# Performance work log

Hardware: AMD Instinct MI355X
Metric: run time of the kernel (lower is better)

## Reference

```python
import jax, jax.numpy as jnp
import numpy as np

B, C, INNER, H, W = 32, 256, 128, 32, 32
EPS = 1e-5


def _conv1x1(x, w):
    # x: (B, Cin, H, W); w: (Cout, Cin) -> (B, Cout, H, W)
    return jnp.einsum('bchw,oc->bohw', x, w)


def _attend(q, k, v):
    # q,k: (B, D, H, W); v: (B, C, H, W)
    b, d, h, w = q.shape
    n = h * w
    qf = q.reshape(b, d, n).transpose(0, 2, 1)            # (B, N, D)
    kf = k.reshape(b, d, n).transpose(0, 2, 1)            # (B, N, D)
    vf = v.reshape(b, v.shape[1], n).transpose(0, 2, 1)   # (B, N, C)
    scale = 1.0 / jnp.sqrt(jnp.asarray(d, qf.dtype))
    attn = jax.nn.softmax(jnp.einsum('bnd,bmd->bnm', qf, kf) * scale, axis=-1)
    of = jnp.einsum('bnm,bmc->bnc', attn, vf)             # (B, N, C)
    return of.transpose(0, 2, 1).reshape(b, -1, h, w)


def _layernorm(x, w, b):
    # Normalize over (C, H, W) jointly; affine params broadcast from (C,1,1).
    mu = jnp.mean(x, axis=(1, 2, 3), keepdims=True)
    var = jnp.mean(jnp.square(x - mu), axis=(1, 2, 3), keepdims=True)
    return (x - mu) * jax.lax.rsqrt(var + EPS) * w[None] + b[None]


def setup_inputs() -> dict:
    key = jax.random.key(0)
    ks = jax.random.split(key, 10)
    s = 0.02
    return {
        'fs': jax.random.normal(ks[0], (B, C, H, W), jnp.float32),
        'fi': jax.random.normal(ks[1], (B, C, H, W), jnp.float32),
        'qs_w': jax.random.normal(ks[2], (INNER, C), jnp.float32) * s,
        'ks_w': jax.random.normal(ks[3], (INNER, C), jnp.float32) * s,
        'vs_w': jax.random.normal(ks[4], (C, C), jnp.float32) * s,
        'qi_w': jax.random.normal(ks[5], (INNER, C), jnp.float32) * s,
        'ki_w': jax.random.normal(ks[6], (INNER, C), jnp.float32) * s,
        'vi_w': jax.random.normal(ks[7], (C, C), jnp.float32) * s,
        'fuse_w': jax.random.normal(ks[8], (C, 2 * C), jnp.float32) * s,
        'fuse_b': jnp.zeros((C,), jnp.float32),
        'ln_s_w': jnp.ones((C, 1, 1), jnp.float32),
        'ln_s_b': jnp.zeros((C, 1, 1), jnp.float32),
        'ln_i_w': jnp.ones((C, 1, 1), jnp.float32),
        'ln_i_b': jnp.zeros((C, 1, 1), jnp.float32),
    }


def reference(fs, fi, qs_w, ks_w, vs_w, qi_w, ki_w, vi_w,
              fuse_w, fuse_b, ln_s_w, ln_s_b, ln_i_w, ln_i_b):
    # sketch queries attend over image keys/values
    s2i = _attend(_conv1x1(fs, qs_w), _conv1x1(fi, ki_w), _conv1x1(fi, vi_w))
    # image queries attend over sketch keys/values
    i2s = _attend(_conv1x1(fi, qi_w), _conv1x1(fs, ks_w), _conv1x1(fs, vs_w))

    def fuse(x):
        return jax.nn.relu(_conv1x1(x, fuse_w) + fuse_b[None, :, None, None])

    fs_out = _layernorm(fuse(jnp.concatenate([fs, i2s], axis=1)) + fs, ln_s_w, ln_s_b)
    fi_out = _layernorm(fuse(jnp.concatenate([fi, s2i], axis=1)) + fi, ln_i_w, ln_i_b)
    return (fs_out, fi_out)
```

## Files before the change

### kernel.cpp

```cpp
#include <hip/hip_runtime.h>

typedef unsigned short u16;
typedef unsigned int   u32;

#define B_   32
#define C_   256
#define N_   1024
#define CN_  (C_*N_)
#define EPS_ 1e-5f

typedef __attribute__((ext_vector_type(8))) short  short8;
typedef __attribute__((ext_vector_type(4))) float  f32x4;

__device__ __forceinline__ float b2f(u16 u){
  union { u32 u; float f; } c; c.u = ((u32)u) << 16; return c.f;
}
__device__ __forceinline__ u16 f2b(float f){
  union { float f; u32 u; } c; c.f = f;
  u32 u = c.u;
  return (u16)((u + 0x7FFFu + ((u >> 16) & 1u)) >> 16);
}

struct F4v { float v[4]; };

__device__ __forceinline__ F4v ld4g(const void* p, long i, int bf){
  F4v r;
  if (bf){
    ushort4 u = *(const ushort4*)((const u16*)p + i);
    r.v[0]=b2f(u.x); r.v[1]=b2f(u.y); r.v[2]=b2f(u.z); r.v[3]=b2f(u.w);
  } else {
    float4 f = *(const float4*)((const float*)p + i);
    r.v[0]=f.x; r.v[1]=f.y; r.v[2]=f.z; r.v[3]=f.w;
  }
  return r;
}
__device__ __forceinline__ float ld1g(const void* p, long i, int bf){
  return bf ? b2f(((const u16*)p)[i]) : ((const float*)p)[i];
}
__device__ __forceinline__ void st1g(void* p, long i, float v, int bf){
  if (bf) ((u16*)p)[i] = f2b(v); else ((float*)p)[i] = v;
}
__device__ __forceinline__ void st4g(void* p, long i, const float* v, int bf){
  if (bf){
    ushort4 u;
    u.x=f2b(v[0]); u.y=f2b(v[1]); u.z=f2b(v[2]); u.w=f2b(v[3]);
    *(ushort4*)((u16*)p + i) = u;
  } else {
    *(float4*)((float*)p + i) = make_float4(v[0],v[1],v[2],v[3]);
  }
}
__device__ __forceinline__ int sniff_bf(const void* lnw){
  return (*(const u32*)lnw == 0x3F803F80u) ? 1 : 0;
}

__global__ __launch_bounds__(256) void k_prep_w(
    const void* qs, const void* ks, const void* vs,
    const void* qi, const void* ki, const void* vi,
    const void* fw, const void* lnw,
    u16* __restrict__ Wcat, u16* __restrict__ fuseWb, float* __restrict__ stats)
{
  const int bf = sniff_bf(lnw);
  if (blockIdx.x == 0 && threadIdx.x < 128) stats[threadIdx.x] = 0.0f;
  const long idx = ((long)blockIdx.x*256 + threadIdx.x) * 4;
  if (idx < 262144){
    const int side = (int)(idx >> 17);
    const int rem  = (int)(idx & 131071);
    const int row  = rem >> 8, col = rem & 255;
    const void* src; int r2;
    if (row < 128)      { src = side ? qi : qs; r2 = row; }
    else if (row < 256) { src = side ? ki : ks; r2 = row - 128; }
    else                { src = side ? vi : vs; r2 = row - 256; }
    F4v v = ld4g(src, (long)r2*256 + col, bf);
    ushort4 u; u.x=f2b(v.v[0]); u.y=f2b(v.v[1]); u.z=f2b(v.v[2]); u.w=f2b(v.v[3]);
    *(ushort4*)&Wcat[idx] = u;
  } else {
    const long j = idx - 262144;
    F4v v = ld4g(fw, j, bf);
    ushort4 u; u.x=f2b(v.v[0]); u.y=f2b(v.v[1]); u.z=f2b(v.v[2]); u.w=f2b(v.v[3]);
    *(ushort4*)&fuseWb[j] = u;
  }
}

__global__ __launch_bounds__(256) void k_prep_t(
    const void* fs, const void* fi, const void* lnw, u16* __restrict__ Ft)
{
  const int bf = sniff_bf(lnw);
  const int nt = blockIdx.x, ct = blockIdx.y, bs = blockIdx.z;
  const int b = bs >> 1, side = bs & 1;
  const void* F = side ? fi : fs;
  const int t = threadIdx.x;
  __shared__ u16 T[64][72];
  const int c0 = ct << 6, n0 = nt << 6;
  const int nc = (t & 15) << 2, cl = t >> 4;
  #pragma unroll
  for (int p = 0; p < 4; p++){
    const int c = cl + (p << 4);
    F4v v = ld4g(F, ((long)b*C_ + c0 + c)*N_ + n0 + nc, bf);
    T[nc  ][c] = f2b(v.v[0]);
    T[nc+1][c] = f2b(v.v[1]);
    T[nc+2][c] = f2b(v.v[2]);
    T[nc+3][c] = f2b(v.v[3]);
  }
  __syncthreads();
  const int nl = t >> 2, cc = (t & 3) << 4;
  float4 x0 = *(const float4*)&T[nl][cc];
  float4 x1 = *(const float4*)&T[nl][cc + 8];
  u16* dst = Ft + ((long)bs << 18) + (long)(n0 + nl)*256 + c0 + cc;
  *(float4*)dst = x0;
  *(float4*)(dst + 8) = x1;
}

__global__ __launch_bounds__(256) void k_proj(
    const u16* __restrict__ Wcat, const u16* __restrict__ Ft,
    u16* __restrict__ QKp, u16* __restrict__ Vp)
{
  const int nt = blockIdx.x;
  const int ot = blockIdx.y;
  const int bs = blockIdx.z;
  const int side = bs & 1;
  const int t = threadIdx.x;
  const int wv = t >> 6, li = t & 15, qd = (t >> 4) & 3;
  const int o0 = (ot << 7) + (wv << 5);
  const int n0 = nt << 7;

  const u16* ap = Wcat + ((long)side*512 + o0 + li)*256 + qd*8;
  const u16* bp = Ft + ((long)bs << 18) + (long)(n0 + li)*256 + qd*8;

  const f32x4 z4 = {0.f,0.f,0.f,0.f};
  f32x4 acc[2][8];
  #pragma unroll
  for (int i = 0; i < 2; i++)
    #pragma unroll
    for (int j = 0; j < 8; j++) acc[i][j] = z4;

  for (int ks = 0; ks < 8; ks++){
    const int ko = ks*32;
    short8 a0 = *(const short8*)(ap + ko);
    short8 a1 = *(const short8*)(ap + 16*256 + ko);
    short8 bfr[8];
    #pragma unroll
    for (int j = 0; j < 8; j++) bfr[j] = *(const short8*)(bp + (long)j*16*256 + ko);
    #pragma unroll
    for (int j = 0; j < 8; j++){
      acc[0][j] = __builtin_amdgcn_mfma_f32_16x16x32_bf16(a0, bfr[j], acc[0][j], 0, 0, 0);
      acc[1][j] = __builtin_amdgcn_mfma_f32_16x16x32_bf16(a1, bfr[j], acc[1][j], 0, 0, 0);
    }
  }

  if (o0 < 256){
    u16* base = QKp + ((long)bs << 18);
    #pragma unroll
    for (int mi = 0; mi < 2; mi++){
      const int ocol = o0 + mi*16 + qd*4;
      #pragma unroll
      for (int j = 0; j < 8; j++){
        const int n = n0 + j*16 + li;
        ushort4 u;
        u.x = f2b(acc[mi][j][0]); u.y = f2b(acc[mi][j][1]);
        u.z = f2b(acc[mi][j][2]); u.w = f2b(acc[mi][j][3]);
        *(ushort4*)&base[(long)n*256 + ocol] = u;
      }
    }
  } else {
    u16* base = Vp + ((long)bs << 18);
    #pragma unroll
    for (int mi = 0; mi < 2; mi++){
      #pragma unroll
      for (int j = 0; j < 8; j++){
        const int n = n0 + j*16 + li;
        #pragma unroll
        for (int r = 0; r < 4; r++){
          const int c = o0 - 256 + mi*16 + qd*4 + r;
          base[(long)c*N_ + n] = f2b(acc[mi][j][r]);
        }
      }
    }
  }
}

#define ATTN_STEP(MT, KCUR, KNXT)                                              \
{                                                                              \
  const int m0s = (MT) << 6;                                                   \
                       \
  short8 va[8];                                                                \
  {                                                                            \
    const u16* vrow = Vb + (long)(cb + li)*N_ + m0s + qd*8;                    \
    _Pragma("unroll")                                                          \
    for (int i4 = 0; i4 < 4; i4++){                                            \
      va[i4*2  ] = *(const short8*)(vrow + (long)i4*16*N_);                    \
      va[i4*2+1] = *(const short8*)(vrow + (long)i4*16*N_ + 32);               \
    }                                                                          \
  }                                                                            \
                  \
  {                                                                            \
    const int m0n = (((MT)+1) & 15) << 6;                                      \
    const u16* krow = Kb + (long)(m0n + (wv<<4) + li)*256 + qd*8;              \
    _Pragma("unroll")                                                          \
    for (int kk = 0; kk < 4; kk++)                                             \
      KNXT[kk] = *(const short8*)(krow + kk*32);                               \
  }                                                                            \
                                \
  f32x4 sf[4];                                                                 \
  sf[0]=z4; sf[1]=z4; sf[2]=z4; sf[3]=z4;                                      \
  _Pragma("unroll")                                                            \
  for (int j4 = 0; j4 < 4; j4++)                                               \
    _Pragma("unroll")                                                          \
    for (int kk = 0; kk < 4; kk++)                                             \
      sf[j4] = __builtin_amdgcn_mfma_f32_16x16x32_bf16(qf[j4][kk], KCUR[kk], sf[j4], 0, 0, 0); \
                  \
  u16 (*Pb)[72] = Pt[(MT) & 1];                                                \
  _Pragma("unroll")                                                            \
  for (int j4 = 0; j4 < 4; j4++){                                              \
    _Pragma("unroll")                                                          \
    for (int r = 0; r < 4; r++){                                               \
      float p = __expf(fminf(sf[j4][r]*scale, 60.0f));                         \
      Pb[(j4<<4) + (qd<<2) + r][(wv<<4) + li] = f2b(p);                        \
      rs[j4][r] += p;                                                          \
    }                                                                          \
  }                                                                            \
  __syncthreads();                                                             \
                                            \
  _Pragma("unroll")                                                            \
  for (int j4 = 0; j4 < 4; j4++){                                              \
    short8 pb0 = *(const short8*)&Pb[(j4<<4) + li][qd*8];                      \
    short8 pb1 = *(const short8*)&Pb[(j4<<4) + li][qd*8 + 32];                 \
    _Pragma("unroll")                                                          \
    for (int i4 = 0; i4 < 4; i4++){                                            \
      accO[i4][j4] = __builtin_amdgcn_mfma_f32_16x16x32_bf16(va[i4*2  ], pb0, accO[i4][j4], 0, 0, 0); \
      accO[i4][j4] = __builtin_amdgcn_mfma_f32_16x16x32_bf16(va[i4*2+1], pb1, accO[i4][j4], 0, 0, 0); \
    }                                                                          \
  }                                                                            \
}

__global__ __launch_bounds__(256) void k_attn(
    const u16* __restrict__ QKp, const u16* __restrict__ Vp, u16* __restrict__ AOt)
{
  const int id   = blockIdx.x;
  const int pair = id & 63;
  const int nt   = id >> 6;
  const int b  = pair >> 1, tt = pair & 1;
  const int qside = 1 - tt, kvside = tt;
  const u16* Qb = QKp + (((long)(b*2+qside)) << 18);
  const u16* Kb = QKp + (((long)(b*2+kvside)) << 18) + 128;
  const u16* Vb = Vp  + (((long)(b*2+kvside)) << 18);

  const int t  = threadIdx.x;
  const int wv = t >> 6;
  const int li = t & 15;
  const int qd = (t >> 4) & 3;
  const int n0 = nt << 6;
  const int cb = wv << 6;

  __shared__ __align__(16) u16 Pt[2][64][72];
  __shared__ float lSp[4][64];

  short8 qf[4][4];
  #pragma unroll
  for (int j4 = 0; j4 < 4; j4++){
    const u16* qrow = Qb + (long)(n0 + (j4<<4) + li)*256 + qd*8;
    #pragma unroll
    for (int kk = 0; kk < 4; kk++) qf[j4][kk] = *(const short8*)(qrow + kk*32);
  }

  const f32x4 z4 = {0.f, 0.f, 0.f, 0.f};
  f32x4 accO[4][4];
  #pragma unroll
  for (int i = 0; i < 4; i++)
    #pragma unroll
    for (int j = 0; j < 4; j++) accO[i][j] = z4;
  float rs[4][4];
  #pragma unroll
  for (int i = 0; i < 4; i++)
    #pragma unroll
    for (int r = 0; r < 4; r++) rs[i][r] = 0.0f;
  const float scale = 0.088388347648318447f;

  short8 kfA[4], kfB[4];
  {
    const u16* krow = Kb + (long)((wv<<4) + li)*256 + qd*8;
    #pragma unroll
    for (int kk = 0; kk < 4; kk++) kfA[kk] = *(const short8*)(krow + kk*32);
  }

  for (int mt2 = 0; mt2 < 16; mt2 += 2){
    ATTN_STEP(mt2,     kfA, kfB)
    ATTN_STEP(mt2 + 1, kfB, kfA)
  }

  #pragma unroll
  for (int j4 = 0; j4 < 4; j4++){
    #pragma unroll
    for (int r = 0; r < 4; r++){
      float s = rs[j4][r];
      s += __shfl_xor(s, 1, 64);
      s += __shfl_xor(s, 2, 64);
      s += __shfl_xor(s, 4, 64);
      s += __shfl_xor(s, 8, 64);
      if (li == 0) lSp[wv][(j4<<4) + (qd<<2) + r] = s;
    }
  }
  __syncthreads();
  float linv[4];
  #pragma unroll
  for (int j4 = 0; j4 < 4; j4++){
    const int q = (j4<<4) + li;
    linv[j4] = 1.0f / (lSp[0][q] + lSp[1][q] + lSp[2][q] + lSp[3][q]);
  }
  u16* aob = AOt + (((long)(b*2+tt)) << 18);
  #pragma unroll
  for (int i4 = 0; i4 < 4; i4++){
    #pragma unroll
    for (int j4 = 0; j4 < 4; j4++){
      const int n = n0 + (j4<<4) + li;
      ushort4 u;
      u.x = f2b(accO[i4][j4][0] * linv[j4]);
      u.y = f2b(accO[i4][j4][1] * linv[j4]);
      u.z = f2b(accO[i4][j4][2] * linv[j4]);
      u.w = f2b(accO[i4][j4][3] * linv[j4]);
      *(ushort4*)&aob[(long)n*256 + cb + (i4<<4) + (qd<<2)] = u;
    }
  }
}

__global__ __launch_bounds__(256) void k_fuse(
    const void* fs, const void* fi, const u16* __restrict__ fuseWb,
    const void* fbias, const u16* __restrict__ Ft, const u16* __restrict__ AOt,
    void* out, float* __restrict__ stats, const void* lnw)
{
  const int bf = sniff_bf(lnw);
  const int nt = blockIdx.x;
  const int ot = blockIdx.y;
  const int bw = blockIdx.z;
  const int b = bw >> 1, w = bw & 1;
  const void* F = w ? fi : fs;
  const int t = threadIdx.x;
  const int wv = t >> 6, li = t & 15, qd = (t >> 4) & 3;
  const int o0 = (ot << 7) + (wv << 5);
  const int n0 = nt << 7;

  const u16* ap  = fuseWb + (long)(o0 + li)*512 + qd*8;
  const u16* bp1 = Ft  + ((long)bw << 18) + (long)(n0 + li)*256 + qd*8;
  const u16* bp2 = AOt + ((long)bw << 18) + (long)(n0 + li)*256 + qd*8;

  const f32x4 z4 = {0.f,0.f,0.f,0.f};
  f32x4 acc[2][8];
  #pragma unroll
  for (int i = 0; i < 2; i++)
    #pragma unroll
    for (int j = 0; j < 8; j++) acc[i][j] = z4;

  for (int ks = 0; ks < 16; ks++){
    const u16* bp = (ks < 8) ? (bp1 + ks*32) : (bp2 + (ks-8)*32);
    const int ko = ks*32;
    short8 a0 = *(const short8*)(ap + ko);
    short8 a1 = *(const short8*)(ap + 16*512 + ko);
    short8 bfr[8];
    #pragma unroll
    for (int j = 0; j < 8; j++) bfr[j] = *(const short8*)(bp + (long)j*16*256);
    #pragma unroll
    for (int j = 0; j < 8; j++){
      acc[0][j] = __builtin_amdgcn_mfma_f32_16x16x32_bf16(a0, bfr[j], acc[0][j], 0, 0, 0);
      acc[1][j] = __builtin_amdgcn_mfma_f32_16x16x32_bf16(a1, bfr[j], acc[1][j], 0, 0, 0);
    }
  }

  __shared__ float rbuf[8];
  float s1 = 0.0f, s2 = 0.0f;
  #pragma unroll
  for (int mi = 0; mi < 2; mi++){
    float biasv[4];
    #pragma unroll
    for (int r = 0; r < 4; r++) biasv[r] = ld1g(fbias, o0 + mi*16 + qd*4 + r, bf);
    #pragma unroll
    for (int j = 0; j < 8; j++){
      const int n = n0 + j*16 + li;
      #pragma unroll
      for (int r = 0; r < 4; r++){
        const int o = o0 + mi*16 + qd*4 + r;
        const float res = ld1g(F, ((long)b*C_ + o)*N_ + n, bf);
        float y = acc[mi][j][r] + biasv[r];
        y = y > 0.0f ? y : 0.0f;
        y += res;
        s1 += y; s2 += y*y;
        st1g(out, ((long)w*B_ + b)*CN_ + (long)o*N_ + n, y, bf);
      }
    }
  }
  #pragma unroll
  for (int off = 32; off > 0; off >>= 1){
    s1 += __shfl_down(s1, off, 64);
    s2 += __shfl_down(s2, off, 64);
  }
  const int lane = t & 63;
  if (lane == 0){ rbuf[wv*2] = s1; rbuf[wv*2+1] = s2; }
  __syncthreads();
  if (t == 0){
    atomicAdd(&stats[bw*2  ], rbuf[0]+rbuf[2]+rbuf[4]+rbuf[6]);
    atomicAdd(&stats[bw*2+1], rbuf[1]+rbuf[3]+rbuf[5]+rbuf[7]);
  }
}

__global__ __launch_bounds__(256) void k_ln(
    void* out, const float* __restrict__ stats,
    const void* lsw, const void* lsb, const void* liw, const void* lib)
{
  const int bf = sniff_bf(lsw);
  const long g = ((long)blockIdx.x*256 + threadIdx.x) * 4;
  const long half = (long)B_*CN_;
  const int w = (g >= half) ? 1 : 0;
  const long rem = g - (long)w*half;
  const int b  = (int)(rem >> 18);
  const int cn = (int)(rem & (CN_-1));
  const int c  = cn >> 10;
  const float s1v = stats[(b*2+w)*2], s2v = stats[(b*2+w)*2+1];
  const float inv = 1.0f / (float)CN_;
  const float mean = s1v * inv;
  const float var  = s2v * inv - mean*mean;
  const float rstd = rsqrtf(var + EPS_);
  const float lw = ld1g(w ? liw : lsw, c, bf);
  const float lb = ld1g(w ? lib : lsb, c, bf);
  F4v x = ld4g(out, g, bf);
  float vv[4];
  #pragma unroll
  for (int j = 0; j < 4; j++) vv[j] = (x.v[j] - mean)*rstd*lw + lb;
  st4g(out, g, vv, bf);
}

extern "C" void kernel_launch(void* const* d_in, const int* in_sizes, int n_in,
                              void* d_out, int out_size, void* d_ws, size_t ws_size,
                              hipStream_t stream)
{
  const void* fs     = d_in[0];
  const void* fi     = d_in[1];
  const void* qs_w   = d_in[2];
  const void* ks_w   = d_in[3];
  const void* vs_w   = d_in[4];
  const void* qi_w   = d_in[5];
  const void* ki_w   = d_in[6];
  const void* vi_w   = d_in[7];
  const void* fuse_w = d_in[8];
  const void* fuse_b = d_in[9];
  const void* ln_s_w = d_in[10];
  const void* ln_s_b = d_in[11];
  const void* ln_i_w = d_in[12];
  const void* ln_i_b = d_in[13];

  char* ws = (char*)d_ws;
  float* stats  = (float*)ws;
  u16*   Wcat   = (u16*)(ws + 4096);
  u16*   fuseWb = (u16*)(ws + 4096 + 524288);
  u16*   Ft     = (u16*)(ws + (1u<<20));
  u16*   QKp    = (u16*)(ws + (1u<<20) + (1u<<25));
  u16*   Vp     = (u16*)(ws + (1u<<20) + 2u*(1u<<25));
  u16*   AOt    = (u16*)(ws + (1u<<20) + 3u*(1u<<25));

  k_prep_w<<<dim3(384), dim3(256), 0, stream>>>(
      qs_w, ks_w, vs_w, qi_w, ki_w, vi_w, fuse_w, ln_s_w, Wcat, fuseWb, stats);
  k_prep_t<<<dim3(16,4,64), dim3(256), 0, stream>>>(fs, fi, ln_s_w, Ft);
  k_proj<<<dim3(8,4,64), dim3(256), 0, stream>>>(Wcat, Ft, QKp, Vp);
  k_attn<<<dim3(1024), dim3(256), 0, stream>>>(QKp, Vp, AOt);
  k_fuse<<<dim3(8,2,64), dim3(256), 0, stream>>>(
      fs, fi, fuseWb, fuse_b, Ft, AOt, d_out, stats, ln_s_w);
  k_ln<<<dim3(16384), dim3(256), 0, stream>>>(
      d_out, stats, ln_s_w, ln_s_b, ln_i_w, ln_i_b);
}
```

Before: 479.8 us.

## Stage V projection stores via LDS and restructure attention loop for occupancy

The projection kernel now stages V-output tiles in shared memory and writes them back with coalesced 16-byte row stores, replacing the strided scalar transposed stores. The attention kernel stops keeping Q fragments in registers and reloads them each tile, which drops the K double buffering. It also adds launch bounds for 3 blocks per CU and remaps block ids so neighbouring blocks share a batch pair. On top of that it uses exp2 with a prescaled constant, packed bf16 conversion, s_setprio around the MFMA sections, and a raw waitcnt+barrier. The goal is higher occupancy and better memory coalescing, at the cost of repeated Q loads from global/cache and an extra LDS buffer in the projection kernel.

```diff
diff --git a/kernel.cpp b/kernel.cpp
--- a/kernel.cpp
+++ b/kernel.cpp
@@ -123,6 +123,8 @@
   const int o0 = (ot << 7) + (wv << 5);
   const int n0 = nt << 7;
 
+  __shared__ __align__(16) u16 VT[128][136];
+
   const u16* ap = Wcat + ((long)side*512 + o0 + li)*256 + qd*8;
   const u16* bp = Ft + ((long)bs << 18) + (long)(n0 + li)*256 + qd*8;
 
@@ -162,82 +164,39 @@
       }
     }
   } else {
-    u16* base = Vp + ((long)bs << 18);
     #pragma unroll
     for (int mi = 0; mi < 2; mi++){
       #pragma unroll
       for (int j = 0; j < 8; j++){
-        const int n = n0 + j*16 + li;
+        const int n = j*16 + li;
         #pragma unroll
         for (int r = 0; r < 4; r++){
-          const int c = o0 - 256 + mi*16 + qd*4 + r;
-          base[(long)c*N_ + n] = f2b(acc[mi][j][r]);
+          const int cl = (wv<<5) + mi*16 + qd*4 + r;
+          VT[cl][n] = f2b(acc[mi][j][r]);
         }
       }
     }
-  }
-}
-
-#define ATTN_STEP(MT, KCUR, KNXT)                                              \
-{                                                                              \
-  const int m0s = (MT) << 6;                                                   \
-                       \
-  short8 va[8];                                                                \
-  {                                                                            \
-    const u16* vrow = Vb + (long)(cb + li)*N_ + m0s + qd*8;                    \
-    _Pragma("unroll")                                                          \
-    for (int i4 = 0; i4 < 4; i4++){                                            \
-      va[i4*2  ] = *(const short8*)(vrow + (long)i4*16*N_);                    \
-      va[i4*2+1] = *(const short8*)(vrow + (long)i4*16*N_ + 32);               \
-    }                                                                          \
-  }                                                                            \
-                  \
-  {                                                                            \
-    const int m0n = (((MT)+1) & 15) << 6;                                      \
-    const u16* krow = Kb + (long)(m0n + (wv<<4) + li)*256 + qd*8;              \
-    _Pragma("unroll")                                                          \
-    for (int kk = 0; kk < 4; kk++)                                             \
-      KNXT[kk] = *(const short8*)(krow + kk*32);                               \
-  }                                                                            \
-                                \
-  f32x4 sf[4];                                                                 \
-  sf[0]=z4; sf[1]=z4; sf[2]=z4; sf[3]=z4;                                      \
-  _Pragma("unroll")                                                            \
-  for (int j4 = 0; j4 < 4; j4++)                                               \
-    _Pragma("unroll")                                                          \
-    for (int kk = 0; kk < 4; kk++)                                             \
-      sf[j4] = __builtin_amdgcn_mfma_f32_16x16x32_bf16(qf[j4][kk], KCUR[kk], sf[j4], 0, 0, 0); \
-                  \
-  u16 (*Pb)[72] = Pt[(MT) & 1];                                                \
-  _Pragma("unroll")                                                            \
-  for (int j4 = 0; j4 < 4; j4++){                                              \
-    _Pragma("unroll")                                                          \
-    for (int r = 0; r < 4; r++){                                               \
-      float p = __expf(fminf(sf[j4][r]*scale, 60.0f));                         \
-      Pb[(j4<<4) + (qd<<2) + r][(wv<<4) + li] = f2b(p);                        \
-      rs[j4][r] += p;                                                          \
-    }                                                                          \
-  }                                                                            \
-  __syncthreads();                                                             \
-                                            \
-  _Pragma("unroll")                                                            \
-  for (int j4 = 0; j4 < 4; j4++){                                              \
-    short8 pb0 = *(const short8*)&Pb[(j4<<4) + li][qd*8];                      \
-    short8 pb1 = *(const short8*)&Pb[(j4<<4) + li][qd*8 + 32];                 \
-    _Pragma("unroll")                                                          \
-    for (int i4 = 0; i4 < 4; i4++){                                            \
-      accO[i4][j4] = __builtin_amdgcn_mfma_f32_16x16x32_bf16(va[i4*2  ], pb0, accO[i4][j4], 0, 0, 0); \
-      accO[i4][j4] = __builtin_amdgcn_mfma_f32_16x16x32_bf16(va[i4*2+1], pb1, accO[i4][j4], 0, 0, 0); \
-    }                                                                          \
-  }                                                                            \
-}
-
-__global__ __launch_bounds__(256) void k_attn(
+    __syncthreads();
+    const int c0g = (ot - 2) << 7;
+    u16* baseV = Vp + ((long)bs << 18);
+    const int rb   = t >> 4;
+    const int c16  = t & 15;
+    #pragma unroll
+    for (int ch = 0; ch < 8; ch++){
+      const int r = rb + (ch << 4);
+      float4 x = *(const float4*)&VT[r][c16*8];
+      *(float4*)&baseV[(long)(c0g + r)*N_ + n0 + c16*8] = x;
+    }
+  }
+}
+
+__global__ __launch_bounds__(256, 3) void k_attn(
     const u16* __restrict__ QKp, const u16* __restrict__ Vp, u16* __restrict__ AOt)
 {
   const int id   = blockIdx.x;
-  const int pair = id & 63;
-  const int nt   = id >> 6;
+  const int loc  = id >> 3;
+  const int pair = ((id & 7) << 3) | (loc >> 4);
+  const int nt   = loc & 15;
   const int b  = pair >> 1, tt = pair & 1;
   const int qside = 1 - tt, kvside = tt;
   const u16* Qb = QKp + (((long)(b*2+qside)) << 18);
@@ -254,13 +213,9 @@
   __shared__ __align__(16) u16 Pt[2][64][72];
   __shared__ float lSp[4][64];
 
-  short8 qf[4][4];
-  #pragma unroll
-  for (int j4 = 0; j4 < 4; j4++){
-    const u16* qrow = Qb + (long)(n0 + (j4<<4) + li)*256 + qd*8;
-    #pragma unroll
-    for (int kk = 0; kk < 4; kk++) qf[j4][kk] = *(const short8*)(qrow + kk*32);
-  }
+  const u16* qbase = Qb + (long)(n0 + li)*256 + qd*8;
+  const u16* kbase = Kb + (long)((wv<<4) + li)*256 + qd*8;
+  const u16* vbase = Vb + (long)(cb + li)*N_ + qd*8;
 
   const f32x4 z4 = {0.f, 0.f, 0.f, 0.f};
   f32x4 accO[4][4];
@@ -273,18 +228,82 @@
   for (int i = 0; i < 4; i++)
     #pragma unroll
     for (int r = 0; r < 4; r++) rs[i][r] = 0.0f;
-  const float scale = 0.088388347648318447f;
-
-  short8 kfA[4], kfB[4];
-  {
-    const u16* krow = Kb + (long)((wv<<4) + li)*256 + qd*8;
-    #pragma unroll
-    for (int kk = 0; kk < 4; kk++) kfA[kk] = *(const short8*)(krow + kk*32);
-  }
-
-  for (int mt2 = 0; mt2 < 16; mt2 += 2){
-    ATTN_STEP(mt2,     kfA, kfB)
-    ATTN_STEP(mt2 + 1, kfB, kfA)
+  const float scale2 = 0.12751742f;
+
+  #pragma unroll 2
+  for (int mt = 0; mt < 16; ++mt){
+    short8 kfc[4];
+    #pragma unroll
+    for (int kk = 0; kk < 4; kk++)
+      kfc[kk] = *(const short8*)(kbase + (long)mt*16384 + kk*32);
+    short8 qA[4], qB[4];
+    #pragma unroll
+    for (int kk = 0; kk < 4; kk++) qA[kk] = *(const short8*)(qbase + kk*32);
+    #pragma unroll
+    for (int kk = 0; kk < 4; kk++) qB[kk] = *(const short8*)(qbase + 4096 + kk*32);
+
+    f32x4 sf[4];
+    sf[0]=z4; sf[1]=z4; sf[2]=z4; sf[3]=z4;
+    __builtin_amdgcn_s_setprio(1);
+    #pragma unroll
+    for (int kk = 0; kk < 4; kk++)
+      sf[0] = __builtin_amdgcn_mfma_f32_16x16x32_bf16(qA[kk], kfc[kk], sf[0], 0, 0, 0);
+    #pragma unroll
+    for (int kk = 0; kk < 4; kk++) qA[kk] = *(const short8*)(qbase + 2*4096 + kk*32);
+    #pragma unroll
+    for (int kk = 0; kk < 4; kk++)
+      sf[1] = __builtin_amdgcn_mfma_f32_16x16x32_bf16(qB[kk], kfc[kk], sf[1], 0, 0, 0);
+    #pragma unroll
+    for (int kk = 0; kk < 4; kk++) qB[kk] = *(const short8*)(qbase + 3*4096 + kk*32);
+    #pragma unroll
+    for (int kk = 0; kk < 4; kk++)
+      sf[2] = __builtin_amdgcn_mfma_f32_16x16x32_bf16(qA[kk], kfc[kk], sf[2], 0, 0, 0);
+    #pragma unroll
+    for (int kk = 0; kk < 4; kk++)
+      sf[3] = __builtin_amdgcn_mfma_f32_16x16x32_bf16(qB[kk], kfc[kk], sf[3], 0, 0, 0);
+    __builtin_amdgcn_s_setprio(0);
+
+    short8 va[8];
+    #pragma unroll
+    for (int i4 = 0; i4 < 4; i4++){
+      va[i4*2  ] = *(const short8*)(vbase + (long)i4*16*N_ + mt*64);
+      va[i4*2+1] = *(const short8*)(vbase + (long)i4*16*N_ + mt*64 + 32);
+    }
+
+    u16 (*Pb)[72] = Pt[mt & 1];
+    #pragma unroll
+    for (int j4 = 0; j4 < 4; j4++){
+      float p0 = exp2f(fminf(sf[j4][0]*scale2, 86.0f));
+      float p1 = exp2f(fminf(sf[j4][1]*scale2, 86.0f));
+      float p2 = exp2f(fminf(sf[j4][2]*scale2, 86.0f));
+      float p3 = exp2f(fminf(sf[j4][3]*scale2, 86.0f));
+      rs[j4][0] += p0; rs[j4][1] += p1;
+      rs[j4][2] += p2; rs[j4][3] += p3;
+      u32 pk0, pk1;
+      asm("v_cvt_pk_bf16_f32 %0, %1, %2" : "=v"(pk0) : "v"(p0), "v"(p1));
+      asm("v_cvt_pk_bf16_f32 %0, %1, %2" : "=v"(pk1) : "v"(p2), "v"(p3));
+      const int rb  = (j4<<4) + (qd<<2);
+      const int col = (wv<<4) + li;
+      Pb[rb  ][col] = (u16)(pk0 & 0xFFFFu);
+      Pb[rb+1][col] = (u16)(pk0 >> 16);
+      Pb[rb+2][col] = (u16)(pk1 & 0xFFFFu);
+      Pb[rb+3][col] = (u16)(pk1 >> 16);
+    }
+
+    asm volatile("s_waitcnt lgkmcnt(0)\n\ts_barrier" ::: "memory");
+
+    __builtin_amdgcn_s_setprio(1);
+    #pragma unroll
+    for (int j4 = 0; j4 < 4; j4++){
+      short8 pb0 = *(const short8*)&Pb[(j4<<4) + li][qd*8];
+      short8 pb1 = *(const short8*)&Pb[(j4<<4) + li][qd*8 + 32];
+      #pragma unroll
+      for (int i4 = 0; i4 < 4; i4++){
+        accO[i4][j4] = __builtin_amdgcn_mfma_f32_16x16x32_bf16(va[i4*2  ], pb0, accO[i4][j4], 0, 0, 0);
+        accO[i4][j4] = __builtin_amdgcn_mfma_f32_16x16x32_bf16(va[i4*2+1], pb1, accO[i4][j4], 0, 0, 0);
+      }
+    }
+    __builtin_amdgcn_s_setprio(0);
   }
 
   #pragma unroll
```

Result: slower. 654.5 us (+36.4%).
